# Optimization experiments

Measured on AMD Instinct MI355X. Metric: run time of the kernel, lower is better.

Reference implementation:

```python
import jax, jax.numpy as jnp
import numpy as np

EMBED_DIM = 1024
NUM_HEADS = 16
HEAD_DIM = EMBED_DIM // NUM_HEADS


def setup_inputs() -> dict:
    key = jax.random.key(0)
    ks = jax.random.split(key, 9)
    B, T, D = 2, 4096, EMBED_DIM
    scale = 1.0 / np.sqrt(D)
    x = jax.random.normal(ks[0], (B, T, D), dtype=jnp.float32)
    # nn.Linear weights stored as (out, in); we use (in, out) layout via transpose-free init
    Wq = jax.random.uniform(ks[1], (D, D), dtype=jnp.float32, minval=-scale, maxval=scale)
    Wk = jax.random.uniform(ks[2], (D, D), dtype=jnp.float32, minval=-scale, maxval=scale)
    Wv = jax.random.uniform(ks[3], (D, D), dtype=jnp.float32, minval=-scale, maxval=scale)
    Wo = jax.random.uniform(ks[4], (D, D), dtype=jnp.float32, minval=-scale, maxval=scale)
    bq = jax.random.uniform(ks[5], (D,), dtype=jnp.float32, minval=-scale, maxval=scale)
    bk = jax.random.uniform(ks[6], (D,), dtype=jnp.float32, minval=-scale, maxval=scale)
    bv = jax.random.uniform(ks[7], (D,), dtype=jnp.float32, minval=-scale, maxval=scale)
    bo = jax.random.uniform(ks[8], (D,), dtype=jnp.float32, minval=-scale, maxval=scale)
    return {"x": x, "Wq": Wq, "bq": bq, "Wk": Wk, "bk": bk,
            "Wv": Wv, "bv": bv, "Wo": Wo, "bo": bo}


def reference(x, Wq, bq, Wk, bk, Wv, bv, Wo, bo):
    B, T, D = x.shape
    H, Hd = NUM_HEADS, HEAD_DIM
    q = x @ Wq + bq  # [B,T,D]
    k = x @ Wk + bk
    v = x @ Wv + bv
    # [B,T,D] -> [B,H,T,Hd]
    q = q.reshape(B, T, H, Hd).transpose(0, 2, 1, 3)
    k = k.reshape(B, T, H, Hd).transpose(0, 2, 1, 3)
    v = v.reshape(B, T, H, Hd).transpose(0, 2, 1, 3)
    att = jnp.einsum('bhqd,bhkd->bhqk', q, k) / jnp.sqrt(jnp.float32(Hd))
    causal = jnp.tril(jnp.ones((T, T), dtype=bool))  # True = keep
    att = jnp.where(causal, att, -jnp.inf)
    att = jax.nn.softmax(att, axis=-1)
    out = jnp.einsum('bhqk,bhkd->bhqd', att, v)  # [B,H,T,Hd]
    out = out.transpose(0, 2, 1, 3).reshape(B, T, D)
    return out @ Wo + bo
```

## Files before the change

kernel.cpp:

```cpp
#include <hip/hip_runtime.h>
#include <hip/hip_bf16.h>
#include <math.h>

typedef __bf16 bf16;
typedef __attribute__((ext_vector_type(8))) __bf16 bf16x8;
typedef __attribute__((ext_vector_type(4))) __bf16 bf16x4;
typedef __attribute__((ext_vector_type(4))) short short4v;
typedef __attribute__((ext_vector_type(4))) float f32x4;

#define MFMA16(a,b,c)  __builtin_amdgcn_mfma_f32_16x16x32_bf16((a),(b),(c),0,0,0)
#define MFMAK16(a,b,c) __builtin_amdgcn_mfma_f32_16x16x16bf16_1k((a),(b),(c),0,0,0)

__device__ __forceinline__ void gload16(const void* gp, void* lp) {
  __builtin_amdgcn_global_load_lds(
      (const __attribute__((address_space(1))) void*)gp,
      (__attribute__((address_space(3))) void*)lp, 16, 0, 0);
}

__global__ __launch_bounds__(256) void cast_x(
    const float* __restrict__ x, bf16* __restrict__ xb)
{
  size_t i = ((size_t)blockIdx.x*256 + threadIdx.x) * 8;
  f32x4 a = *(const f32x4*)(x+i);
  f32x4 b = *(const f32x4*)(x+i+4);
  bf16x8 o;
  #pragma unroll
  for (int j=0;j<4;j++) { o[j] = (bf16)a[j]; o[4+j] = (bf16)b[j]; }
  *(bf16x8*)(xb+i) = o;
}

__global__ __launch_bounds__(1024) void tr_cast(
    const float* __restrict__ w0, const float* __restrict__ w1,
    const float* __restrict__ w2, bf16* __restrict__ dst)
{
  __shared__ bf16 tile[64][65];
  const float* src = (blockIdx.z==0)?w0:(blockIdx.z==1)?w1:w2;
  bf16* d = dst + (size_t)blockIdx.z * (1024*1024);
  int x = threadIdx.x, y = threadIdx.y;
  int tc = blockIdx.x, tr = blockIdx.y;
  #pragma unroll
  for (int i=0;i<4;i++) {
    int r = y + i*16;
    tile[r][x] = (bf16)src[(size_t)(tr*64+r)*1024 + tc*64 + x];
  }
  __syncthreads();
  #pragma unroll
  for (int i=0;i<4;i++) {
    int r = y + i*16;
    d[(size_t)(tc*64+r)*1024 + tr*64 + x] = tile[x][r];
  }
}

__global__ __launch_bounds__(1024) void v_tr(
    const bf16* __restrict__ v, bf16* __restrict__ vt)
{
  __shared__ bf16 tile[64][65];
  int x = threadIdx.x, y = threadIdx.y;
  int tt = blockIdx.x;
  int bh = blockIdx.y;
  int b = bh >> 4, h = bh & 15;
  const bf16* src = v + ((size_t)b*4096 + tt*64)*1024 + h*64;
  bf16* dst = vt + ((size_t)bh*64)*4096 + tt*64;
  #pragma unroll
  for (int i=0;i<4;i++) {
    int r = y + i*16;
    tile[r][x] = src[(size_t)r*1024 + x];
  }
  __syncthreads();
  #pragma unroll
  for (int i=0;i<4;i++) {
    int r = y + i*16;
    dst[(size_t)r*4096 + x] = tile[x][r];
  }
}

__global__ __launch_bounds__(256) void gemm_qkv(
    const bf16* __restrict__ A, const bf16* __restrict__ Bt,
    const float* __restrict__ bq, const float* __restrict__ bk, const float* __restrict__ bv,
    bf16* __restrict__ q, bf16* __restrict__ k, bf16* __restrict__ v,
    int M, int K)
{
  __shared__ __align__(16) bf16 As[128*32];
  __shared__ __align__(16) bf16 Bs[128*32];
  const int tid  = threadIdx.x;
  const int wave = tid >> 6;
  const int lane = tid & 63;
  const int l15  = lane & 15;
  const int quad = lane >> 4;
  const int m0 = blockIdx.y * 128;
  const int n0 = blockIdx.x * 128;
  const int wm = (wave >> 1) * 64;
  const int wn = (wave & 1) * 64;
  const int srow = lane >> 2;
  const int scol = (lane & 3) * 8;

  f32x4 acc[4][4];
  #pragma unroll
  for (int i=0;i<4;i++)
    #pragma unroll
    for (int j=0;j<4;j++)
      acc[i][j] = (f32x4){0.f,0.f,0.f,0.f};

  for (int k0 = 0; k0 < K; k0 += 32) {
    __syncthreads();
    #pragma unroll
    for (int p=0;p<2;p++) {
      int c = p*4 + wave;
      int row = c*16 + srow;
      gload16(A  + (size_t)(m0+row)*K + k0 + scol, As + c*512);
      gload16(Bt + (size_t)(n0+row)*K + k0 + scol, Bs + c*512);
    }
    __syncthreads();
    bf16x8 af[4], bfr[4];
    #pragma unroll
    for (int t=0;t<4;t++) {
      af[t]  = *(const bf16x8*)(As + (wm + t*16 + l15)*32 + quad*8);
      bfr[t] = *(const bf16x8*)(Bs + (wn + t*16 + l15)*32 + quad*8);
    }
    #pragma unroll
    for (int mt=0;mt<4;mt++)
      #pragma unroll
      for (int nt=0;nt<4;nt++)
        acc[mt][nt] = MFMA16(af[mt], bfr[nt], acc[mt][nt]);
  }

  const int mat = n0 >> 10;
  const float* bsel = (mat==0) ? bq : (mat==1) ? bk : bv;
  bf16*       osel  = (mat==0) ? q  : (mat==1) ? k  : v;
  const float qsc   = (mat==0) ? 0.1803368801f : 1.0f;
  #pragma unroll
  for (int nt=0;nt<4;nt++) {
    int col = n0 + wn + nt*16 + l15;
    int cw  = col & 1023;
    float bvv = bsel[cw];
    #pragma unroll
    for (int mt=0;mt<4;mt++) {
      int row = m0 + wm + mt*16 + quad*4;
      #pragma unroll
      for (int r=0;r<4;r++)
        osel[(size_t)(row + r)*1024 + cw] = (bf16)((acc[mt][nt][r] + bvv) * qsc);
    }
  }
}

__global__ __launch_bounds__(256, 4) void gemm_out(
    const bf16* __restrict__ A, const bf16* __restrict__ Bt,
    const float* __restrict__ bias, float* __restrict__ C,
    int M, int N, int K)
{
  __shared__ __align__(16) bf16 As[128*32];
  __shared__ __align__(16) bf16 Bs[64*32];
  const int tid  = threadIdx.x;
  const int wave = tid >> 6;
  const int lane = tid & 63;
  const int l15  = lane & 15;
  const int quad = lane >> 4;
  const int m0 = blockIdx.y * 128;
  const int n0 = blockIdx.x * 64;
  const int wm = (wave >> 1) * 64;
  const int wn = (wave & 1) * 32;
  const int srow = lane >> 2;
  const int scol = (lane & 3) * 8;

  f32x4 acc[4][2];
  #pragma unroll
  for (int i=0;i<4;i++)
    #pragma unroll
    for (int j=0;j<2;j++)
      acc[i][j] = (f32x4){0.f,0.f,0.f,0.f};

  for (int k0 = 0; k0 < K; k0 += 32) {
    __syncthreads();
    #pragma unroll
    for (int p=0;p<2;p++) {
      int c = p*4 + wave;
      int row = c*16 + srow;
      gload16(A + (size_t)(m0+row)*K + k0 + scol, As + c*512);
    }
    {
      int row = wave*16 + srow;
      gload16(Bt + (size_t)(n0+row)*K + k0 + scol, Bs + wave*512);
    }
    __syncthreads();
    bf16x8 af[4], bfr[2];
    #pragma unroll
    for (int t=0;t<4;t++)
      af[t]  = *(const bf16x8*)(As + (wm + t*16 + l15)*32 + quad*8);
    #pragma unroll
    for (int t=0;t<2;t++)
      bfr[t] = *(const bf16x8*)(Bs + (wn + t*16 + l15)*32 + quad*8);
    #pragma unroll
    for (int mt=0;mt<4;mt++)
      #pragma unroll
      for (int nt=0;nt<2;nt++)
        acc[mt][nt] = MFMA16(af[mt], bfr[nt], acc[mt][nt]);
  }

  #pragma unroll
  for (int nt=0;nt<2;nt++) {
    int col = n0 + wn + nt*16 + l15;
    float bvv = bias[col];
    #pragma unroll
    for (int mt=0;mt<4;mt++) {
      int row = m0 + wm + mt*16 + quad*4;
      #pragma unroll
      for (int r=0;r<4;r++)
        C[(size_t)(row + r)*N + col] = acc[mt][nt][r] + bvv;
    }
  }
}

__global__ __launch_bounds__(256, 2) void attn_fwd(
    const bf16* __restrict__ Q, const bf16* __restrict__ Kp,
    const bf16* __restrict__ Vtg, bf16* __restrict__ O)
{
  __shared__ __align__(16) char KsB[2*8192];
  __shared__ __align__(16) char VtB[2*8192];

  const int tid  = threadIdx.x;
  const int w    = tid >> 6;
  const int lane = tid & 63;
  const int l15  = lane & 15;
  const int quad = lane >> 4;

  const int bid = blockIdx.x;
  const int pp  = bid >> 5;
  const int bh  = bid & 31;
  const int h   = bh & 15;
  const int b   = bh >> 4;

  const size_t headoff = (size_t)h * 64;
  const size_t bbase   = (size_t)b * 4096;

  short4v ones_s;
  {
    bf16x4 o1;
    #pragma unroll
    for (int j=0;j<4;j++) o1[j] = (bf16)1.0f;
    ones_s = __builtin_bit_cast(short4v, o1);
  }

  const int kt_row = tid >> 2;
  const int kswz   = (kt_row & 7) << 4;
  const int ks_w0  = kt_row*128 + (((tid & 3)*32)      ^ kswz);
  const int ks_w1  = kt_row*128 + (((tid & 3)*32 + 16) ^ kswz);

  const int vd  = tid >> 2;
  const int vt0 = (tid & 3) * 16;
  int vw[4];
  #pragma unroll
  for (int u=0;u<4;u++)
    vw[u] = vd*128 + (((vt0 + u*4)*2) ^ ((vd & 15) << 3));

  const int s7    = l15 & 7;
  const int ks_r0 = l15*128 + ((quad ^ (s7 & 3)) << 4) + ((s7 >> 2) << 6);
  const int ks_r1 = ks_r0 ^ 64;
  const int vt_rbase = l15*128 + ((quad ^ (l15 & 3)) << 3) + ((l15 >> 2) << 5);
  int vt_r[4];
  #pragma unroll
  for (int tt=0;tt<4;tt++) vt_r[tt] = vt_rbase ^ (tt << 5);

  const bf16* kbase0 = Kp  + (bbase + kt_row)*1024 + headoff + (tid & 3)*16;
  const bf16* vbase0 = Vtg + ((size_t)(bh*64) + vd)*4096 + vt0;

  for (int ph = 0; ph < 2; ++ph) {
    const int qt = ph ? (31 - pp) : pp;
    const int q0 = qt * 128;
    const int ktmax = 2*qt + 1;

    bf16x8 aqA[2], aqB[2];
    {
      int rowA = q0 + w*16 + l15;
      const bf16* qp = Q + (bbase + rowA)*1024 + headoff + quad*8;
      aqA[0] = *(const bf16x8*)(qp);
      aqA[1] = *(const bf16x8*)(qp + 32);
      qp += 64*1024;
      aqB[0] = *(const bf16x8*)(qp);
      aqB[1] = *(const bf16x8*)(qp + 32);
    }

    f32x4 accoA[4], accoB[4], accliA, accliB;
    #pragma unroll
    for (int i=0;i<4;i++) { accoA[i] = (f32x4){0.f,0.f,0.f,0.f}; accoB[i] = (f32x4){0.f,0.f,0.f,0.f}; }
    accliA = (f32x4){0.f,0.f,0.f,0.f};
    accliB = (f32x4){0.f,0.f,0.f,0.f};

    __syncthreads();
    {
      bf16x8 k0 = *(const bf16x8*)(kbase0);
      bf16x8 k1 = *(const bf16x8*)(kbase0 + 8);
      *(bf16x8*)(KsB + ks_w0) = k0;
      *(bf16x8*)(KsB + ks_w1) = k1;
      bf16x8 v0 = *(const bf16x8*)(vbase0);
      bf16x8 v1 = *(const bf16x8*)(vbase0 + 8);
      *(bf16x4*)(VtB + vw[0]) = __builtin_shufflevector(v0, v0, 0,1,2,3);
      *(bf16x4*)(VtB + vw[1]) = __builtin_shufflevector(v0, v0, 4,5,6,7);
      *(bf16x4*)(VtB + vw[2]) = __builtin_shufflevector(v1, v1, 0,1,2,3);
      *(bf16x4*)(VtB + vw[3]) = __builtin_shufflevector(v1, v1, 4,5,6,7);
    }
    __syncthreads();

    const bf16* kpref = kbase0 + 64*1024;
    const bf16* vpref = vbase0 + 64;

    for (int kt = 0; kt <= ktmax; ++kt) {
      const int p = kt & 1;
      const bool pre = (kt < ktmax);

      bf16x8 kr0, kr1, vr0, vr1;
      if (pre) {
        kr0 = *(const bf16x8*)(kpref);
        kr1 = *(const bf16x8*)(kpref + 8);
        vr0 = *(const bf16x8*)(vpref);
        vr1 = *(const bf16x8*)(vpref + 8);
        kpref += 64*1024;
        vpref += 64;
      }

      const char* ksb = KsB + p*8192;
      const char* vtb = VtB + p*8192;

      f32x4 accsA[4], accsB[4];
      #pragma unroll
      for (int i=0;i<4;i++) { accsA[i] = (f32x4){0.f,0.f,0.f,0.f}; accsB[i] = (f32x4){0.f,0.f,0.f,0.f}; }

      __builtin_amdgcn_s_setprio(1);
      #pragma unroll
      for (int kk=0;kk<2;kk++) {
        #pragma unroll
        for (int tt=0;tt<4;tt++) {
          bf16x8 ka = *(const bf16x8*)(ksb + (kk ? ks_r1 : ks_r0) + tt*2048);
          accsA[tt] = MFMA16(ka, aqA[kk], accsA[tt]);
          accsB[tt] = MFMA16(ka, aqB[kk], accsB[tt]);
        }
      }
      __builtin_amdgcn_s_setprio(0);

      short4v ptsA[4], ptsB[4];
      if (kt < 2*qt) {
        #pragma unroll
        for (int tt=0;tt<4;tt++) {
          bf16x4 pa, pb;
          #pragma unroll
          for (int r=0;r<4;r++) {
            pa[r] = (bf16)__builtin_amdgcn_exp2f(fminf(accsA[tt][r], 60.0f));
            pb[r] = (bf16)__builtin_amdgcn_exp2f(fminf(accsB[tt][r], 60.0f));
          }
          ptsA[tt] = __builtin_bit_cast(short4v, pa);
          ptsB[tt] = __builtin_bit_cast(short4v, pb);
        }
      } else {
        const bool adead = (kt > 2*qt);
        #pragma unroll
        for (int tt=0;tt<4;tt++) {
          bf16x4 pa, pb;
          #pragma unroll
          for (int r=0;r<4;r++) {
            const bool tq = (tt*16 + quad*4 + r > w*16 + l15);
            float fa = __builtin_amdgcn_exp2f(fminf(accsA[tt][r], 60.0f));
            if (adead || tq) fa = 0.0f;
            float fb = __builtin_amdgcn_exp2f(fminf(accsB[tt][r], 60.0f));
            if (adead && tq) fb = 0.0f;
            pa[r] = (bf16)fa; pb[r] = (bf16)fb;
          }
          ptsA[tt] = __builtin_bit_cast(short4v, pa);
          ptsB[tt] = __builtin_bit_cast(short4v, pb);
        }
      }

      __builtin_amdgcn_s_setprio(1);
      #pragma unroll
      for (int nt=0;nt<4;nt++) {
        #pragma unroll
        for (int tt=0;tt<4;tt++) {
          bf16x4 va = *(const bf16x4*)(vtb + vt_r[tt] + nt*2048);
          short4v vas = __builtin_bit_cast(short4v, va);
          accoA[nt] = MFMAK16(vas, ptsA[tt], accoA[nt]);
          accoB[nt] = MFMAK16(vas, ptsB[tt], accoB[nt]);
        }
      }
      #pragma unroll
      for (int tt=0;tt<4;tt++) {
        accliA = MFMAK16(ones_s, ptsA[tt], accliA);
        accliB = MFMAK16(ones_s, ptsB[tt], accliB);
      }
      __builtin_amdgcn_s_setprio(0);

      if (pre) {
        char* ksn = KsB + (p^1)*8192;
        char* vtn = VtB + (p^1)*8192;
        *(bf16x8*)(ksn + ks_w0) = kr0;
        *(bf16x8*)(ksn + ks_w1) = kr1;
        *(bf16x4*)(vtn + vw[0]) = __builtin_shufflevector(vr0, vr0, 0,1,2,3);
        *(bf16x4*)(vtn + vw[1]) = __builtin_shufflevector(vr0, vr0, 4,5,6,7);
        *(bf16x4*)(vtn + vw[2]) = __builtin_shufflevector(vr1, vr1, 0,1,2,3);
        *(bf16x4*)(vtn + vw[3]) = __builtin_shufflevector(vr1, vr1, 4,5,6,7);
        __syncthreads();
      }
    }

    {
      float invA = 1.0f / accliA[0];
      float invB = 1.0f / accliB[0];
      int rowA = q0 + w*16 + l15;
      bf16* obA = O + (bbase + rowA)*1024 + headoff;
      bf16* obB = obA + 64*1024;
      #pragma unroll
      for (int nt=0;nt<4;nt++) {
        bf16x4 oA, oB;
        #pragma unroll
        for (int r=0;r<4;r++) {
          oA[r] = (bf16)(accoA[nt][r] * invA);
          oB[r] = (bf16)(accoB[nt][r] * invB);
        }
        *(bf16x4*)(obA + nt*16 + quad*4) = oA;
        *(bf16x4*)(obB + nt*16 + quad*4) = oB;
      }
    }
  }
}

extern "C" void kernel_launch(void* const* d_in, const int* in_sizes, int n_in,
                              void* d_out, int out_size, void* d_ws, size_t ws_size,
                              hipStream_t stream) {
  const float* x  = (const float*)d_in[0];
  const float* Wq = (const float*)d_in[1];
  const float* bq = (const float*)d_in[2];
  const float* Wk = (const float*)d_in[3];
  const float* bk = (const float*)d_in[4];
  const float* Wv = (const float*)d_in[5];
  const float* bv = (const float*)d_in[6];
  const float* Wo = (const float*)d_in[7];
  const float* bo = (const float*)d_in[8];
  float* out = (float*)d_out;

  bf16* ws = (bf16*)d_ws;
  bf16* q  = ws;
  bf16* k  = q + (size_t)8192*1024;
  bf16* v  = k + (size_t)8192*1024;
  bf16* xb = v + (size_t)8192*1024;
  bf16* ao = q;
  bf16* WtQKV = (bf16*)d_out;
  bf16* vT    = (bf16*)d_out;
  bf16* WtO   = xb;

  tr_cast<<<dim3(16,16,3), dim3(64,16), 0, stream>>>(Wq, Wk, Wv, WtQKV);
  cast_x<<<4096, 256, 0, stream>>>(x, xb);
  gemm_qkv<<<dim3(24,64), 256, 0, stream>>>(xb, WtQKV, bq, bk, bv, q, k, v, 8192, 1024);
  v_tr<<<dim3(64,32), dim3(64,16), 0, stream>>>(v, vT);
  tr_cast<<<dim3(16,16,1), dim3(64,16), 0, stream>>>(Wo, Wo, Wo, WtO);
  attn_fwd<<<512, 256, 0, stream>>>(q, k, vT, ao);
  gemm_out<<<dim3(16,64), 256, 0, stream>>>(ao, WtO, bo, out, 8192, 1024, 1024);
}
```

Measured before the change: 307.7 us.

## Deepen GEMM K-tiles with swizzled LDS and quad-buffer attention K/V pipeline

Both GEMM kernels now stage 64-wide K slices per iteration instead of 32, with an XOR swizzle on the LDS layout to avoid bank conflicts. This halves the number of barrier pairs per GEMM. The attention kernel moves from a double to a four-slot K/V buffer with two tiles in flight, prefetching two ahead and syncing every other iteration. It also drops the fminf clamp before exp2. The changes use more LDS, which may lower occupancy, and removing the clamp relies on the scores staying bounded.

```diff
diff --git a/kernel.cpp b/kernel.cpp
--- a/kernel.cpp
+++ b/kernel.cpp
@@ -80,8 +80,8 @@
     bf16* __restrict__ q, bf16* __restrict__ k, bf16* __restrict__ v,
     int M, int K)
 {
-  __shared__ __align__(16) bf16 As[128*32];
-  __shared__ __align__(16) bf16 Bs[128*32];
+  __shared__ __align__(16) bf16 As[128*64];
+  __shared__ __align__(16) bf16 Bs[128*64];
   const int tid  = threadIdx.x;
   const int wave = tid >> 6;
   const int lane = tid & 63;
@@ -91,8 +91,18 @@
   const int n0 = blockIdx.x * 128;
   const int wm = (wave >> 1) * 64;
   const int wn = (wave & 1) * 64;
-  const int srow = lane >> 2;
-  const int scol = (lane & 3) * 8;
+
+  int srow[4], scol[4];
+  #pragma unroll
+  for (int p=0;p<4;p++) {
+    int cid = p*256 + tid;
+    srow[p] = cid >> 3;
+    scol[p] = ((cid & 7) ^ (srow[p] & 7)) << 3;
+  }
+  const int swz8 = l15 & 7;
+  int rdo[2];
+  #pragma unroll
+  for (int kk=0;kk<2;kk++) rdo[kk] = (((kk*4 + quad) ^ swz8) << 3);
 
   f32x4 acc[4][4];
   #pragma unroll
@@ -101,27 +111,29 @@
     for (int j=0;j<4;j++)
       acc[i][j] = (f32x4){0.f,0.f,0.f,0.f};
 
-  for (int k0 = 0; k0 < K; k0 += 32) {
-    __syncthreads();
-    #pragma unroll
-    for (int p=0;p<2;p++) {
-      int c = p*4 + wave;
-      int row = c*16 + srow;
-      gload16(A  + (size_t)(m0+row)*K + k0 + scol, As + c*512);
-      gload16(Bt + (size_t)(n0+row)*K + k0 + scol, Bs + c*512);
-    }
-    __syncthreads();
-    bf16x8 af[4], bfr[4];
-    #pragma unroll
-    for (int t=0;t<4;t++) {
-      af[t]  = *(const bf16x8*)(As + (wm + t*16 + l15)*32 + quad*8);
-      bfr[t] = *(const bf16x8*)(Bs + (wn + t*16 + l15)*32 + quad*8);
-    }
-    #pragma unroll
-    for (int mt=0;mt<4;mt++)
-      #pragma unroll
-      for (int nt=0;nt<4;nt++)
-        acc[mt][nt] = MFMA16(af[mt], bfr[nt], acc[mt][nt]);
+  for (int k0 = 0; k0 < K; k0 += 64) {
+    __syncthreads();
+    #pragma unroll
+    for (int p=0;p<4;p++) {
+      int cid = p*256 + tid;
+      gload16(A  + (size_t)(m0+srow[p])*K + k0 + scol[p], As + cid*8);
+      gload16(Bt + (size_t)(n0+srow[p])*K + k0 + scol[p], Bs + cid*8);
+    }
+    __syncthreads();
+    #pragma unroll
+    for (int kk=0;kk<2;kk++) {
+      bf16x8 af[4], bfr[4];
+      #pragma unroll
+      for (int t=0;t<4;t++) {
+        af[t]  = *(const bf16x8*)(As + (wm + t*16 + l15)*64 + rdo[kk]);
+        bfr[t] = *(const bf16x8*)(Bs + (wn + t*16 + l15)*64 + rdo[kk]);
+      }
+      #pragma unroll
+      for (int mt=0;mt<4;mt++)
+        #pragma unroll
+        for (int nt=0;nt<4;nt++)
+          acc[mt][nt] = MFMA16(af[mt], bfr[nt], acc[mt][nt]);
+    }
   }
 
   const int mat = n0 >> 10;
@@ -148,8 +160,8 @@
     const float* __restrict__ bias, float* __restrict__ C,
     int M, int N, int K)
 {
-  __shared__ __align__(16) bf16 As[128*32];
-  __shared__ __align__(16) bf16 Bs[64*32];
+  __shared__ __align__(16) bf16 As[128*64];
+  __shared__ __align__(16) bf16 Bs[64*64];
   const int tid  = threadIdx.x;
   const int wave = tid >> 6;
   const int lane = tid & 63;
@@ -159,8 +171,18 @@
   const int n0 = blockIdx.x * 64;
   const int wm = (wave >> 1) * 64;
   const int wn = (wave & 1) * 32;
-  const int srow = lane >> 2;
-  const int scol = (lane & 3) * 8;
+
+  int srow[4], scol[4];
+  #pragma unroll
+  for (int p=0;p<4;p++) {
+    int cid = p*256 + tid;
+    srow[p] = cid >> 3;
+    scol[p] = ((cid & 7) ^ (srow[p] & 7)) << 3;
+  }
+  const int swz8 = l15 & 7;
+  int rdo[2];
+  #pragma unroll
+  for (int kk=0;kk<2;kk++) rdo[kk] = (((kk*4 + quad) ^ swz8) << 3);
 
   f32x4 acc[4][2];
   #pragma unroll
@@ -169,31 +191,32 @@
     for (int j=0;j<2;j++)
       acc[i][j] = (f32x4){0.f,0.f,0.f,0.f};
 
-  for (int k0 = 0; k0 < K; k0 += 32) {
-    __syncthreads();
+  for (int k0 = 0; k0 < K; k0 += 64) {
+    __syncthreads();
+    #pragma unroll
+    for (int p=0;p<4;p++)
+      gload16(A + (size_t)(m0+srow[p])*K + k0 + scol[p], As + (p*256+tid)*8);
     #pragma unroll
     for (int p=0;p<2;p++) {
-      int c = p*4 + wave;
-      int row = c*16 + srow;
-      gload16(A + (size_t)(m0+row)*K + k0 + scol, As + c*512);
-    }
-    {
-      int row = wave*16 + srow;
-      gload16(Bt + (size_t)(n0+row)*K + k0 + scol, Bs + wave*512);
-    }
-    __syncthreads();
-    bf16x8 af[4], bfr[2];
-    #pragma unroll
-    for (int t=0;t<4;t++)
-      af[t]  = *(const bf16x8*)(As + (wm + t*16 + l15)*32 + quad*8);
-    #pragma unroll
-    for (int t=0;t<2;t++)
-      bfr[t] = *(const bf16x8*)(Bs + (wn + t*16 + l15)*32 + quad*8);
-    #pragma unroll
-    for (int mt=0;mt<4;mt++)
-      #pragma unroll
-      for (int nt=0;nt<2;nt++)
-        acc[mt][nt] = MFMA16(af[mt], bfr[nt], acc[mt][nt]);
+      int cid = p*256 + tid;
+      gload16(Bt + (size_t)(n0+srow[p])*K + k0 + scol[p], Bs + cid*8);
+    }
+    __syncthreads();
+    #pragma unroll
+    for (int kk=0;kk<2;kk++) {
+      bf16x8 af[4], bfr[2];
+      #pragma unroll
+      for (int t=0;t<4;t++)
+        af[t]  = *(const bf16x8*)(As + (wm + t*16 + l15)*64 + rdo[kk]);
+      #pragma unroll
+      for (int t=0;t<2;t++)
+        bfr[t] = *(const bf16x8*)(Bs + (wn + t*16 + l15)*64 + rdo[kk]);
+      #pragma unroll
+      for (int mt=0;mt<4;mt++)
+        #pragma unroll
+        for (int nt=0;nt<2;nt++)
+          acc[mt][nt] = MFMA16(af[mt], bfr[nt], acc[mt][nt]);
+    }
   }
 
   #pragma unroll
@@ -214,8 +237,8 @@
     const bf16* __restrict__ Q, const bf16* __restrict__ Kp,
     const bf16* __restrict__ Vtg, bf16* __restrict__ O)
 {
-  __shared__ __align__(16) char KsB[2*8192];
-  __shared__ __align__(16) char VtB[2*8192];
+  __shared__ __align__(16) char KsB[4*8192];
+  __shared__ __align__(16) char VtB[4*8192];
 
   const int tid  = threadIdx.x;
   const int w    = tid >> 6;
@@ -286,26 +309,30 @@
     accliB = (f32x4){0.f,0.f,0.f,0.f};
 
     __syncthreads();
-    {
-      bf16x8 k0 = *(const bf16x8*)(kbase0);
-      bf16x8 k1 = *(const bf16x8*)(kbase0 + 8);
-      *(bf16x8*)(KsB + ks_w0) = k0;
-      *(bf16x8*)(KsB + ks_w1) = k1;
-      bf16x8 v0 = *(const bf16x8*)(vbase0);
-      bf16x8 v1 = *(const bf16x8*)(vbase0 + 8);
-      *(bf16x4*)(VtB + vw[0]) = __builtin_shufflevector(v0, v0, 0,1,2,3);
-      *(bf16x4*)(VtB + vw[1]) = __builtin_shufflevector(v0, v0, 4,5,6,7);
-      *(bf16x4*)(VtB + vw[2]) = __builtin_shufflevector(v1, v1, 0,1,2,3);
-      *(bf16x4*)(VtB + vw[3]) = __builtin_shufflevector(v1, v1, 4,5,6,7);
-    }
-    __syncthreads();
-
-    const bf16* kpref = kbase0 + 64*1024;
-    const bf16* vpref = vbase0 + 64;
+    #pragma unroll
+    for (int j=0;j<2;j++) {
+      const bf16* kp = kbase0 + (size_t)j*64*1024;
+      const bf16* vp = vbase0 + j*64;
+      bf16x8 k0 = *(const bf16x8*)(kp);
+      bf16x8 k1 = *(const bf16x8*)(kp + 8);
+      bf16x8 v0 = *(const bf16x8*)(vp);
+      bf16x8 v1 = *(const bf16x8*)(vp + 8);
+      char* ksn = KsB + j*8192;
+      char* vtn = VtB + j*8192;
+      *(bf16x8*)(ksn + ks_w0) = k0;
+      *(bf16x8*)(ksn + ks_w1) = k1;
+      *(bf16x4*)(vtn + vw[0]) = __builtin_shufflevector(v0, v0, 0,1,2,3);
+      *(bf16x4*)(vtn + vw[1]) = __builtin_shufflevector(v0, v0, 4,5,6,7);
+      *(bf16x4*)(vtn + vw[2]) = __builtin_shufflevector(v1, v1, 0,1,2,3);
+      *(bf16x4*)(vtn + vw[3]) = __builtin_shufflevector(v1, v1, 4,5,6,7);
+    }
+    __syncthreads();
+
+    const bf16* kpref = kbase0 + (size_t)2*64*1024;
+    const bf16* vpref = vbase0 + 128;
 
     for (int kt = 0; kt <= ktmax; ++kt) {
-      const int p = kt & 1;
-      const bool pre = (kt < ktmax);
+      const bool pre = (kt + 2 <= ktmax);
 
       bf16x8 kr0, kr1, vr0, vr1;
       if (pre) {
@@ -317,8 +344,8 @@
         vpref += 64;
       }
 
-      const char* ksb = KsB + p*8192;
-      const char* vtb = VtB + p*8192;
+      const char* ksb = KsB + (kt & 3)*8192;
+      const char* vtb = VtB + (kt & 3)*8192;
 
       f32x4 accsA[4], accsB[4];
       #pragma unroll
@@ -343,8 +370,8 @@
           bf16x4 pa, pb;
           #pragma unroll
           for (int r=0;r<4;r++) {
-            pa[r] = (bf16)__builtin_amdgcn_exp2f(fminf(accsA[tt][r], 60.0f));
-            pb[r] = (bf16)__builtin_amdgcn_exp2f(fminf(accsB[tt][r], 60.0f));
+            pa[r] = (bf16)__builtin_amdgcn_exp2f(accsA[tt][r]);
+            pb[r] = (bf16)__builtin_amdgcn_exp2f(accsB[tt][r]);
           }
           ptsA[tt] = __builtin_bit_cast(short4v, pa);
           ptsB[tt] = __builtin_bit_cast(short4v, pb);
@@ -357,9 +384,9 @@
           #pragma unroll
           for (int r=0;r<4;r++) {
             const bool tq = (tt*16 + quad*4 + r > w*16 + l15);
-            float fa = __builtin_amdgcn_exp2f(fminf(accsA[tt][r], 60.0f));
+            float fa = __builtin_amdgcn_exp2f(accsA[tt][r]);
             if (adead || tq) fa = 0.0f;
-            float fb = __builtin_amdgcn_exp2f(fminf(accsB[tt][r], 60.0f));
+            float fb = __builtin_amdgcn_exp2f(accsB[tt][r]);
             if (adead && tq) fb = 0.0f;
             pa[r] = (bf16)fa; pb[r] = (bf16)fb;
           }
@@ -387,16 +414,16 @@
       __builtin_amdgcn_s_setprio(0);
 
       if (pre) {
-        char* ksn = KsB + (p^1)*8192;
-        char* vtn = VtB + (p^1)*8192;
+        char* ksn = KsB + ((kt + 2) & 3)*8192;
+        char* vtn = VtB + ((kt + 2) & 3)*8192;
         *(bf16x8*)(ksn + ks_w0) = kr0;
         *(bf16x8*)(ksn + ks_w1) = kr1;
         *(bf16x4*)(vtn + vw[0]) = __builtin_shufflevector(vr0, vr0, 0,1,2,3);
         *(bf16x4*)(vtn + vw[1]) = __builtin_shufflevector(vr0, vr0, 4,5,6,7);
         *(bf16x4*)(vtn + vw[2]) = __builtin_shufflevector(vr1, vr1, 0,1,2,3);
         *(bf16x4*)(vtn + vw[3]) = __builtin_shufflevector(vr1, vr1, 4,5,6,7);
-        __syncthreads();
-      }
+      }
+      if (kt & 1) __syncthreads();
     }
 
     {
```

Measured after the change: 295.7 us, median of 3. 3.9% less time.
